# Performance work log

Measured on AMD Instinct MI355X. Metric: run time of the kernel, lower is better.

## Reference

```python
import jax, jax.numpy as jnp
import numpy as np

ALPHA_MAX = 0.1


def setup_inputs() -> dict:
    key = jax.random.key(0)
    ks = jax.random.split(key, 9)
    B, M, L = 256, 3, 100000
    A, H = 4096, 512
    return {
        "x": jax.random.uniform(ks[0], (B, M, L), dtype=jnp.float32),  # log1p scores, non-negative
        "active_idx": jax.random.randint(ks[1], (A,), 0, L, dtype=jnp.int64 if jax.config.jax_enable_x64 else jnp.int32),
        "global_logits": jnp.log(jnp.full((M,), 1.0 / M, dtype=jnp.float32) + 1e-12),
        "delta_w": 0.01 * jax.random.normal(ks[2], (M, L), dtype=jnp.float32),
        "bias": 0.01 * jax.random.normal(ks[3], (L,), dtype=jnp.float32),
        "log_alpha": jnp.float32(-3.0),
        "hidden_w": jax.random.normal(ks[4], (H, M * A), dtype=jnp.float32) * (1.0 / np.sqrt(M * A)),
        "hidden_b": 0.01 * jax.random.normal(ks[5], (H,), dtype=jnp.float32),
        "delta_layer_w": jax.random.normal(ks[6], (A, H), dtype=jnp.float32) * (1.0 / np.sqrt(H)),
        "delta_layer_b": 0.01 * jax.random.normal(ks[7], (A,), dtype=jnp.float32),
    }


def reference(x, active_idx, global_logits, delta_w, bias, log_alpha,
              hidden_w, hidden_b, delta_layer_w, delta_layer_b):
    B = x.shape[0]
    # base logits: elementwise weighted sum over the 3 models, per-label weights
    w_eff = jax.nn.softmax(global_logits)[:, None] + delta_w          # (M, L)
    logits = jnp.einsum("bml,ml->bl", x, w_eff) + bias                # (B, L)
    # gather active labels -> 2-layer MLP (dropout is identity in eval)
    x_active = x[:, :, active_idx].reshape(B, -1)                     # (B, M*A)
    h = jax.nn.relu(x_active @ hidden_w.T + hidden_b)                 # (B, H)
    delta_active = h @ delta_layer_w.T + delta_layer_b                # (B, A)
    # scaled scatter-add back into full logits (duplicates accumulate)
    alpha = ALPHA_MAX * jax.nn.sigmoid(log_alpha)
    logits = logits.at[:, active_idx].add(alpha * delta_active)
    return logits
```

## Files before the change

### kernel.cpp

```cpp
#include <hip/hip_runtime.h>
#include <math.h>

#define B_ 256
#define M_ 3
#define L_ 100000
#define A_ 4096
#define H_ 512
#define MA_ (M_*A_)
#define K1_ MA_
#define NZ_ 8
#define KC1_ (K1_/NZ_)
#define BCHUNK_ 4
#define LITER_ 4

#define NWIN_    98
#define NB_HW_   3072
#define NB_W2_   1024
#define NB_CVT_  (NB_HW_+NB_W2_)
#define NB_LGX_  25
#define NB_LG_   (NB_LGX_*(B_/BCHUNK_))

typedef __attribute__((ext_vector_type(8))) short bf16x8;
typedef __attribute__((ext_vector_type(8))) unsigned short u16x8;
typedef __attribute__((ext_vector_type(4))) float f32x4;
typedef __attribute__((ext_vector_type(4))) int i32x4;

static __device__ __forceinline__ f32x4 ld4(const float* p) {
    return *reinterpret_cast<const f32x4*>(p);
}
static __device__ __forceinline__ f32x4 ld4nt(const float* p) {
    return __builtin_nontemporal_load(reinterpret_cast<const f32x4*>(p));
}
static __device__ __forceinline__ void st4nt(float* p, f32x4 v) {
    __builtin_nontemporal_store(v, reinterpret_cast<f32x4*>(p));
}
static __device__ __forceinline__ unsigned short f2bf(float f) {
    unsigned u = __float_as_uint(f);
    unsigned r = (u + 0x7FFFu + ((u >> 16) & 1u)) >> 16;
    return (unsigned short)r;
}

__global__ void init_head(int* __restrict__ head) {
    int i = blockIdx.x * blockDim.x + threadIdx.x;
    if (i < L_ / 4) {
        i32x4 m1 = {-1, -1, -1, -1};
        *reinterpret_cast<i32x4*>(head + i * 4) = m1;
    }
}

__global__ void window_hist(const int* __restrict__ idx, int* __restrict__ jbase) {
    __shared__ int cnt[NWIN_];
    for (int w = threadIdx.x; w < NWIN_; w += 256) cnt[w] = 0;
    __syncthreads();
    for (int a = threadIdx.x; a < A_; a += 256) atomicAdd(&cnt[idx[a] >> 10], 1);
    __syncthreads();
    if (threadIdx.x == 0) {
        int s = 0;
        for (int w = 0; w < NWIN_; ++w) { jbase[w] = s; s += cnt[w]; }
        jbase[NWIN_] = s;
    }
}

__global__ void build_perm(const int* __restrict__ idx, const int* __restrict__ jbase,
                           int* __restrict__ a_of_j, int* __restrict__ l_of_j,
                           int* __restrict__ head2) {
    __shared__ int ml[A_];
    __shared__ int ma[A_];
    __shared__ int nm_sh;
    int w = blockIdx.x, tid = threadIdx.x;
    if (tid == 0) nm_sh = 0;
    __syncthreads();
    for (int a = tid; a < A_; a += 256) {
        int l = idx[a];
        if ((l >> 10) == w) { int p = atomicAdd(&nm_sh, 1); ml[p] = l; ma[p] = a; }
    }
    __syncthreads();
    int nm = nm_sh;
    int base = jbase[w];
    for (int p = tid; p < nm; p += 256) {
        int l = ml[p], a = ma[p];
        int rank = 0, same_smaller = 0;
        for (int q = 0; q < nm; ++q) {
            int lq = ml[q], aq = ma[q];
            rank += (lq < l) | ((lq == l) & (aq < a));
            same_smaller += ((lq == l) & (aq < a));
        }
        int j = base + rank;
        a_of_j[j] = a;
        l_of_j[j] = l;
        if (same_smaller == 0) head2[l] = j;
    }
    if (w == 0 && tid == 0) l_of_j[A_] = -1;
}

__global__ __launch_bounds__(256) void mega(
    const float* __restrict__ x, const float* __restrict__ gl,
    const float* __restrict__ dw, const float* __restrict__ bias,
    const int* __restrict__ head2, const int* __restrict__ l_of_j,
    const int* __restrict__ a_of_j,
    float* __restrict__ logits, unsigned short* __restrict__ xa,
    const float* __restrict__ hw, unsigned short* __restrict__ hwb,
    const float* __restrict__ w2, unsigned short* __restrict__ w2b) {
    int bid = blockIdx.x;
    int tid = threadIdx.x;

    if (bid < NB_CVT_) {
        if (bid < NB_HW_) {
            int i = bid * 256 + tid;
            int o = i * 8;
            int n = o / MA_;
            int col = o % MA_;
            int m = col >> 12, j0 = col & (A_ - 1);
            const float* row = hw + (size_t)n * MA_ + (m << 12);
            u16x8 out;
            #pragma unroll
            for (int t = 0; t < 8; ++t) out[t] = f2bf(row[a_of_j[j0 + t]]);
            *reinterpret_cast<u16x8*>(hwb + (size_t)o) = out;
        } else {
            int i = (bid - NB_HW_) * 256 + tid;
            f32x4 v0 = ld4nt(w2 + (size_t)i * 8);
            f32x4 v1 = ld4nt(w2 + (size_t)i * 8 + 4);
            u16x8 o;
            o[0] = f2bf(v0.x); o[1] = f2bf(v0.y); o[2] = f2bf(v0.z); o[3] = f2bf(v0.w);
            o[4] = f2bf(v1.x); o[5] = f2bf(v1.y); o[6] = f2bf(v1.z); o[7] = f2bf(v1.w);
            *reinterpret_cast<u16x8*>(w2b + (size_t)i * 8) = o;
        }
        return;
    }

    const int L4 = L_ / 4;
    int lgbid = bid - NB_CVT_;
    int lblk = lgbid % NB_LGX_;
    int b0 = (lgbid / NB_LGX_) * BCHUNK_;

    float g0 = gl[0], g1 = gl[1], g2 = gl[2];
    float mx = fmaxf(g0, fmaxf(g1, g2));
    float e0 = expf(g0 - mx), e1 = expf(g1 - mx), e2 = expf(g2 - mx);
    float inv = 1.0f / (e0 + e1 + e2);
    float s0 = e0 * inv, s1 = e1 * inv, s2 = e2 * inv;

    #pragma unroll 1
    for (int it = 0; it < LITER_; ++it) {
        int i = lblk * (256 * LITER_) + it * 256 + tid;
        if (i >= L4) continue;
        int l = i * 4;

        f32x4 w0 = ld4(dw + l) + s0;
        f32x4 w1 = ld4(dw + L_ + l) + s1;
        f32x4 w2v = ld4(dw + 2 * L_ + l) + s2;
        f32x4 bb = ld4(bias + l);
        i32x4 heads = *reinterpret_cast<const i32x4*>(head2 + l);

        f32x4 X[BCHUNK_][3];
        #pragma unroll
        for (int c = 0; c < BCHUNK_; ++c) {
            const float* xb = x + (size_t)(b0 + c) * M_ * L_ + l;
            X[c][0] = ld4nt(xb);
            X[c][1] = ld4nt(xb + L_);
            X[c][2] = ld4nt(xb + 2 * L_);
        }
        #pragma unroll
        for (int c = 0; c < BCHUNK_; ++c) {
            f32x4 o = X[c][0] * w0 + X[c][1] * w1 + X[c][2] * w2v + bb;
            st4nt(logits + (size_t)(b0 + c) * L_ + l, o);
        }

        #pragma unroll
        for (int c = 0; c < 4; ++c) {
            int j = heads[c];
            if (j >= 0) {
                int lh = l + c;
                do {
                    #pragma unroll
                    for (int b = 0; b < BCHUNK_; ++b) {
                        unsigned short* xab = xa + (size_t)(b0 + b) * MA_;
                        xab[j]          = f2bf(X[b][0][c]);
                        xab[A_ + j]     = f2bf(X[b][1][c]);
                        xab[2 * A_ + j] = f2bf(X[b][2][c]);
                    }
                    ++j;
                } while (l_of_j[j] == lh);
            }
        }
    }
}

__global__ __launch_bounds__(256) void gemm1_mfma(
    const unsigned short* __restrict__ Xa, const unsigned short* __restrict__ W,
    float* __restrict__ part) {
    int tid = threadIdx.x;
    int wave = tid >> 6, lane = tid & 63;
    int row0 = blockIdx.x * 64 + (wave >> 1) * 32;
    int col0 = blockIdx.y * 64 + (wave & 1) * 32;
    int k0 = blockIdx.z * KC1_;
    int lr = lane & 15;
    int lk = (lane >> 4) * 8;
    const unsigned short* pa0 = Xa + (size_t)(row0 + lr) * K1_ + k0 + lk;
    const unsigned short* pa1 = pa0 + (size_t)16 * K1_;
    const unsigned short* pb0 = W + (size_t)(col0 + lr) * K1_ + k0 + lk;
    const unsigned short* pb1 = pb0 + (size_t)16 * K1_;
    f32x4 acc00 = {0.f,0.f,0.f,0.f}, acc01 = {0.f,0.f,0.f,0.f};
    f32x4 acc10 = {0.f,0.f,0.f,0.f}, acc11 = {0.f,0.f,0.f,0.f};
    #pragma unroll 4
    for (int k = 0; k < KC1_; k += 32) {
        bf16x8 a0 = *reinterpret_cast<const bf16x8*>(pa0 + k);
        bf16x8 a1 = *reinterpret_cast<const bf16x8*>(pa1 + k);
        bf16x8 b0 = *reinterpret_cast<const bf16x8*>(pb0 + k);
        bf16x8 b1 = *reinterpret_cast<const bf16x8*>(pb1 + k);
        acc00 = __builtin_amdgcn_mfma_f32_16x16x32_bf16(a0, b0, acc00, 0, 0, 0);
        acc01 = __builtin_amdgcn_mfma_f32_16x16x32_bf16(a0, b1, acc01, 0, 0, 0);
        acc10 = __builtin_amdgcn_mfma_f32_16x16x32_bf16(a1, b0, acc10, 0, 0, 0);
        acc11 = __builtin_amdgcn_mfma_f32_16x16x32_bf16(a1, b1, acc11, 0, 0, 0);
    }
    float* base = part + (size_t)blockIdx.z * B_ * H_;
    #pragma unroll
    for (int j = 0; j < 4; ++j) {
        int r = (lane >> 4) * 4 + j;
        base[(size_t)(row0 + r) * H_ + col0 + lr]           = acc00[j];
        base[(size_t)(row0 + r) * H_ + col0 + 16 + lr]      = acc01[j];
        base[(size_t)(row0 + 16 + r) * H_ + col0 + lr]      = acc10[j];
        base[(size_t)(row0 + 16 + r) * H_ + col0 + 16 + lr] = acc11[j];
    }
}

__global__ void reduce_relu(const float* __restrict__ part,
                            const float* __restrict__ hb,
                            unsigned short* __restrict__ h) {
    int t = blockIdx.x * blockDim.x + threadIdx.x;
    if (t >= B_ * H_) return;
    int n = t & (H_ - 1);
    float s = hb[n];
    #pragma unroll
    for (int z = 0; z < NZ_; ++z) s += part[(size_t)z * B_ * H_ + t];
    h[t] = f2bf(fmaxf(s, 0.0f));
}

__global__ __launch_bounds__(256) void gemm2_scatter(
    const unsigned short* __restrict__ Hm, const unsigned short* __restrict__ W2,
    const float* __restrict__ b2, const float* __restrict__ la,
    const int* __restrict__ idx, float* __restrict__ logits) {
    int tid = threadIdx.x;
    int wave = tid >> 6, lane = tid & 63;
    int row0 = blockIdx.x * 64 + (wave >> 1) * 32;
    int col0 = blockIdx.y * 64 + (wave & 1) * 32;
    int lr = lane & 15;
    int lk = (lane >> 4) * 8;
    const unsigned short* pa0 = Hm + (size_t)(row0 + lr) * H_ + lk;
    const unsigned short* pa1 = pa0 + (size_t)16 * H_;
    const unsigned short* pb0 = W2 + (size_t)(col0 + lr) * H_ + lk;
    const unsigned short* pb1 = pb0 + (size_t)16 * H_;
    f32x4 acc00 = {0.f,0.f,0.f,0.f}, acc01 = {0.f,0.f,0.f,0.f};
    f32x4 acc10 = {0.f,0.f,0.f,0.f}, acc11 = {0.f,0.f,0.f,0.f};
    #pragma unroll 4
    for (int k = 0; k < H_; k += 32) {
        bf16x8 a0 = *reinterpret_cast<const bf16x8*>(pa0 + k);
        bf16x8 a1 = *reinterpret_cast<const bf16x8*>(pa1 + k);
        bf16x8 b0 = *reinterpret_cast<const bf16x8*>(pb0 + k);
        bf16x8 b1 = *reinterpret_cast<const bf16x8*>(pb1 + k);
        acc00 = __builtin_amdgcn_mfma_f32_16x16x32_bf16(a0, b0, acc00, 0, 0, 0);
        acc01 = __builtin_amdgcn_mfma_f32_16x16x32_bf16(a0, b1, acc01, 0, 0, 0);
        acc10 = __builtin_amdgcn_mfma_f32_16x16x32_bf16(a1, b0, acc10, 0, 0, 0);
        acc11 = __builtin_amdgcn_mfma_f32_16x16x32_bf16(a1, b1, acc11, 0, 0, 0);
    }
    float alpha = 0.1f / (1.0f + expf(-la[0]));
    int c0 = col0 + lr, c1 = col0 + 16 + lr;
    int l0 = idx[c0], l1 = idx[c1];
    float bias0 = b2[c0], bias1 = b2[c1];
    #pragma unroll
    for (int j = 0; j < 4; ++j) {
        int r = (lane >> 4) * 4 + j;
        atomicAdd(&logits[(size_t)(row0 + r) * L_ + l0],      alpha * (acc00[j] + bias0));
        atomicAdd(&logits[(size_t)(row0 + r) * L_ + l1],      alpha * (acc01[j] + bias1));
        atomicAdd(&logits[(size_t)(row0 + 16 + r) * L_ + l0], alpha * (acc10[j] + bias0));
        atomicAdd(&logits[(size_t)(row0 + 16 + r) * L_ + l1], alpha * (acc11[j] + bias1));
    }
}

static inline size_t align256(size_t x) { return (x + 255) & ~(size_t)255; }

extern "C" void kernel_launch(void* const* d_in, const int* in_sizes, int n_in,
                              void* d_out, int out_size, void* d_ws, size_t ws_size,
                              hipStream_t stream) {
    const float* x    = (const float*)d_in[0];
    const int*   idx  = (const int*)d_in[1];
    const float* gl   = (const float*)d_in[2];
    const float* dw   = (const float*)d_in[3];
    const float* bias = (const float*)d_in[4];
    const float* la   = (const float*)d_in[5];
    const float* hw   = (const float*)d_in[6];
    const float* hb   = (const float*)d_in[7];
    const float* w2   = (const float*)d_in[8];
    const float* b2   = (const float*)d_in[9];
    float* logits = (float*)d_out;

    char* ws = (char*)d_ws;
    int* head2 = (int*)ws;                     ws += align256((size_t)L_ * 4);
    int* jbase = (int*)ws;                     ws += align256((size_t)(NWIN_ + 1) * 4);
    int* a_of_j = (int*)ws;                    ws += align256((size_t)A_ * 4);
    int* l_of_j = (int*)ws;                    ws += align256((size_t)(A_ + 1) * 4);
    unsigned short* xa = (unsigned short*)ws;  ws += align256((size_t)B_ * MA_ * 2);
    unsigned short* hwb = (unsigned short*)ws; ws += align256((size_t)H_ * MA_ * 2);
    unsigned short* w2b = (unsigned short*)ws; ws += align256((size_t)A_ * H_ * 2);
    float* part = (float*)ws;                  ws += align256((size_t)NZ_ * B_ * H_ * 4);
    unsigned short* h = (unsigned short*)ws;   ws += align256((size_t)B_ * H_ * 2);

    init_head<<<(L_ / 4 + 255) / 256, 256, 0, stream>>>(head2);
    window_hist<<<1, 256, 0, stream>>>(idx, jbase);
    build_perm<<<NWIN_, 256, 0, stream>>>(idx, jbase, a_of_j, l_of_j, head2);

    mega<<<NB_CVT_ + NB_LG_, 256, 0, stream>>>(
        x, gl, dw, bias, head2, l_of_j, a_of_j, logits, xa, hw, hwb, w2, w2b);

    gemm1_mfma<<<dim3(B_ / 64, H_ / 64, NZ_), 256, 0, stream>>>(xa, hwb, part);
    reduce_relu<<<(B_ * H_ + 255) / 256, 256, 0, stream>>>(part, hb, h);
    gemm2_scatter<<<dim3(B_ / 64, A_ / 64), 256, 0, stream>>>(h, w2b, b2, la, idx, logits);
}
```

Before: 215.5 us.

## Restructure logits kernel to one batch row per block and double GEMM1 split-K

The fused logits/gather kernel switches from blocks that cover four batch rows over a strided L range to blocks that each handle one batch row and a contiguous 4096-label chunk. Each block walks the three models in turn, keeping four vectors in flight per thread, and gathers active labels into the bf16 buffer as it goes. This raises block count and parallelism, but delta_w and bias are now reloaded for every batch row instead of being shared across four. The GEMM1 split-K factor also goes from 8 to 16, which gives more blocks but more partial sums to reduce.

Measured after the change: 453.5 us. 110% more time.

```diff
diff --git a/kernel.cpp b/kernel.cpp
--- a/kernel.cpp
+++ b/kernel.cpp
@@ -8,17 +8,16 @@
 #define H_ 512
 #define MA_ (M_*A_)
 #define K1_ MA_
-#define NZ_ 8
+#define NZ_ 16
 #define KC1_ (K1_/NZ_)
-#define BCHUNK_ 4
-#define LITER_ 4
 
 #define NWIN_    98
 #define NB_HW_   3072
 #define NB_W2_   1024
 #define NB_CVT_  (NB_HW_+NB_W2_)
-#define NB_LGX_  25
-#define NB_LG_   (NB_LGX_*(B_/BCHUNK_))
+#define CH_      4096
+#define NCHUNK_  25
+#define NB_LG_   (NCHUNK_*B_)
 
 typedef __attribute__((ext_vector_type(8))) short bf16x8;
 typedef __attribute__((ext_vector_type(8))) unsigned short u16x8;
@@ -128,60 +127,61 @@
         return;
     }
 
-    const int L4 = L_ / 4;
     int lgbid = bid - NB_CVT_;
-    int lblk = lgbid % NB_LGX_;
-    int b0 = (lgbid / NB_LGX_) * BCHUNK_;
+    int b = lgbid & (B_ - 1);
+    int ch = lgbid >> 8;
+    int l0 = ch * CH_;
 
     float g0 = gl[0], g1 = gl[1], g2 = gl[2];
     float mx = fmaxf(g0, fmaxf(g1, g2));
     float e0 = expf(g0 - mx), e1 = expf(g1 - mx), e2 = expf(g2 - mx);
     float inv = 1.0f / (e0 + e1 + e2);
-    float s0 = e0 * inv, s1 = e1 * inv, s2 = e2 * inv;
-
-    #pragma unroll 1
-    for (int it = 0; it < LITER_; ++it) {
-        int i = lblk * (256 * LITER_) + it * 256 + tid;
-        if (i >= L4) continue;
-        int l = i * 4;
-
-        f32x4 w0 = ld4(dw + l) + s0;
-        f32x4 w1 = ld4(dw + L_ + l) + s1;
-        f32x4 w2v = ld4(dw + 2 * L_ + l) + s2;
-        f32x4 bb = ld4(bias + l);
-        i32x4 heads = *reinterpret_cast<const i32x4*>(head2 + l);
-
-        f32x4 X[BCHUNK_][3];
+    float sm3[3] = {e0 * inv, e1 * inv, e2 * inv};
+
+    const float* xb = x + (size_t)b * (M_ * L_);
+    unsigned short* xab_base = xa + (size_t)b * MA_;
+    f32x4 acc[4];
+
+    #pragma unroll
+    for (int m = 0; m < 3; ++m) {
+        const float* xm = xb + (size_t)m * L_;
+        const float* dm = dw + (size_t)m * L_;
+        float sm = sm3[m];
+        f32x4 xv[4], dv[4];
         #pragma unroll
-        for (int c = 0; c < BCHUNK_; ++c) {
-            const float* xb = x + (size_t)(b0 + c) * M_ * L_ + l;
-            X[c][0] = ld4nt(xb);
-            X[c][1] = ld4nt(xb + L_);
-            X[c][2] = ld4nt(xb + 2 * L_);
+        for (int p = 0; p < 4; ++p) {
+            int l = l0 + (((p << 8) + tid) << 2);
+            if (l < L_) xv[p] = ld4nt(xm + l);
         }
         #pragma unroll
-        for (int c = 0; c < BCHUNK_; ++c) {
-            f32x4 o = X[c][0] * w0 + X[c][1] * w1 + X[c][2] * w2v + bb;
-            st4nt(logits + (size_t)(b0 + c) * L_ + l, o);
-        }
-
+        for (int p = 0; p < 4; ++p) {
+            int l = l0 + (((p << 8) + tid) << 2);
+            if (l < L_) dv[p] = ld4(dm + l);
+        }
+        unsigned short* xab = xab_base + m * A_;
         #pragma unroll
-        for (int c = 0; c < 4; ++c) {
-            int j = heads[c];
-            if (j >= 0) {
-                int lh = l + c;
-                do {
-                    #pragma unroll
-                    for (int b = 0; b < BCHUNK_; ++b) {
-                        unsigned short* xab = xa + (size_t)(b0 + b) * MA_;
-                        xab[j]          = f2bf(X[b][0][c]);
-                        xab[A_ + j]     = f2bf(X[b][1][c]);
-                        xab[2 * A_ + j] = f2bf(X[b][2][c]);
+        for (int p = 0; p < 4; ++p) {
+            int l = l0 + (((p << 8) + tid) << 2);
+            if (l < L_) {
+                f32x4 t = xv[p] * (dv[p] + sm);
+                acc[p] = (m == 0) ? t : (acc[p] + t);
+                i32x4 heads = *reinterpret_cast<const i32x4*>(head2 + l);
+                #pragma unroll
+                for (int c = 0; c < 4; ++c) {
+                    int j = heads[c];
+                    if (j >= 0) {
+                        unsigned short vv = f2bf(xv[p][c]);
+                        int lh = l + c;
+                        do { xab[j] = vv; ++j; } while (l_of_j[j] == lh);
                     }
-                    ++j;
-                } while (l_of_j[j] == lh);
+                }
             }
         }
+    }
+    #pragma unroll
+    for (int p = 0; p < 4; ++p) {
+        int l = l0 + (((p << 8) + tid) << 2);
+        if (l < L_) st4nt(logits + (size_t)b * L_ + l, acc[p] + ld4(bias + l));
     }
 }
 
```
